# Kernel tuning notes

Measured on AMD Instinct MI355X. Metric: run time of the kernel, lower is better.

## Reference

```python
import jax, jax.numpy as jnp
import numpy as np

GRANULARITY = 50
PERCENTILES = (0.01, 0.99)


def setup_inputs() -> dict:
    key = jax.random.key(0)
    H = W = 6144
    sp = jax.random.uniform(key, (H, W), dtype=jnp.float32)
    return {
        "signal_probabilities": sp,
        "rho_max": jnp.float32(H - 1),
        "rho_min": jnp.float32(0.0),
        "theta_min_horizontal": jnp.float32(0.01),
        "theta_max_horizontal": jnp.float32(0.05),
        "theta_min_vertical": jnp.float32(1.52),
        "theta_max_vertical": jnp.float32(1.56),
    }


def _linspace(a, b, n):
    t = jnp.arange(n, dtype=jnp.float32) / (n - 1)
    return a + (b - a) * t


def _fix_edge_effects(buf):
    buf = buf.at[0, :].set(buf[1, :])
    buf = buf.at[-1, :].set(buf[-2, :])
    buf = buf.at[:, 0].set(buf[:, 1])
    buf = buf.at[:, -1].set(buf[:, -2])
    return buf


def _fill_buffer(H, W, thetas, rhos, mode):
    # vectorized over all granularity lines at once (no python loop over lines)
    if mode == "horizontal":
        y = jnp.arange(H)
        # x[g, H]: x = -y*tan(theta) + rho/cos(theta)
        x = -y[None, :] * jnp.tan(thetas)[:, None] + (rhos / jnp.cos(thetas))[:, None]
        x = jnp.clip(jnp.round(x).astype(jnp.int32), 0, W - 1)
        yb = jnp.broadcast_to(y[None, :], x.shape)
        buf = jnp.zeros((H, W), jnp.int32).at[yb, x].add(1)
        buf = jnp.cumsum(buf, axis=1)
    else:
        x = jnp.arange(W)
        # y[g, W]: y = -x/tan(theta) + rho/sin(theta)
        y = -x[None, :] / jnp.tan(thetas)[:, None] + (rhos / jnp.sin(thetas))[:, None]
        y = jnp.clip(jnp.round(y).astype(jnp.int32), 0, H - 1)
        xb = jnp.broadcast_to(x[None, :], y.shape)
        buf = jnp.zeros((H, W), jnp.int32).at[y, xb].add(1)
        buf = jnp.cumsum(buf, axis=0)
    return _fix_edge_effects(buf)


def _get_bounds(nsp, thetas, rhos, mode):
    g = GRANULARITY
    H, W = nsp.shape
    buf = _fill_buffer(H, W, thetas, rhos, mode)
    # segment-sum replaces the dense one_hot * probs reduction (same math)
    values = jax.ops.segment_sum(nsp.reshape(-1), buf.reshape(-1), num_segments=g)
    c = jnp.cumsum(values) / jnp.sum(values)
    lower = jnp.argmax(c >= PERCENTILES[0])  # first index with cumsum >= p0
    upper = (g - 1) - jnp.argmax((c <= PERCENTILES[1])[::-1]) + 2  # last index with cumsum <= p1, +2
    return lower, upper


def _take_neg(a, i):
    # a[-i] with python-style negative indexing (i == 0 -> a[0])
    g = a.shape[0]
    return jnp.take(a, (g - i) % g)


def _intersect(r1, t1, r2, t2):
    det = jnp.cos(t1) * jnp.sin(t2) - jnp.cos(t2) * jnp.sin(t1)
    x = (r1 * jnp.sin(t2) - r2 * jnp.sin(t1)) / det
    y = (r2 * jnp.cos(t1) - r1 * jnp.cos(t2)) / det
    return jnp.stack((x, y))


def reference(signal_probabilities, rho_max, rho_min, theta_min_horizontal,
              theta_max_horizontal, theta_min_vertical, theta_max_vertical):
    g = GRANULARITY
    nsp = signal_probabilities - signal_probabilities.min()
    nsp = nsp / nsp.sum()
    rhos = _linspace(rho_max, rho_min, g)
    th = _linspace(theta_min_horizontal, theta_max_horizontal, g)
    tv = _linspace(theta_min_vertical, theta_max_vertical, g)
    lh, uh = _get_bounds(nsp, th, rhos, "horizontal")
    lv, uv = _get_bounds(nsp, tv, rhos, "vertical")
    r_min_h, r_max_h = _take_neg(rhos, lh), _take_neg(rhos, uh)
    t_min_h, t_max_h = _take_neg(th, lh), _take_neg(th, uh)
    r_min_v, r_max_v = _take_neg(rhos, lv), _take_neg(rhos, uv)
    t_min_v, t_max_v = _take_neg(tv, lv), _take_neg(tv, uv)
    # [top-left, top-right, bottom-right, bottom-left] -> shape (4, 2)
    return jnp.stack([
        _intersect(r_min_h, t_min_h, r_min_v, t_min_v),
        _intersect(r_max_h, t_max_h, r_min_v, t_min_v),
        _intersect(r_max_h, t_max_h, r_max_v, t_max_v),
        _intersect(r_min_h, t_min_h, r_max_v, t_max_v),
    ], axis=0)
```

## Files before the change

### kernel.cpp

```cpp
#include <hip/hip_runtime.h>
#include <math.h>

#define HH 6144
#define WW 6144
constexpr int G = 50;
constexpr int NCOPY = 64;
constexpr int NG = NCOPY * G;
constexpr int BIG = 0x0FFFFFFF;
constexpr int C0 = 4 * NG + NCOPY;


__device__ inline void ldsAddF(float* p, float v)      { __hip_atomic_fetch_add(p, v, __ATOMIC_RELAXED, __HIP_MEMORY_SCOPE_WORKGROUP); }
__device__ inline void ldsAddU(unsigned* p, unsigned v){ __hip_atomic_fetch_add(p, v, __ATOMIC_RELAXED, __HIP_MEMORY_SCOPE_WORKGROUP); }
__device__ inline void glbAddF(float* p, float v)      { __hip_atomic_fetch_add(p, v, __ATOMIC_RELAXED, __HIP_MEMORY_SCOPE_AGENT); }
__device__ inline void glbAddU(unsigned* p, unsigned v){ __hip_atomic_fetch_add(p, v, __ATOMIC_RELAXED, __HIP_MEMORY_SCOPE_AGENT); }

__global__ void crop_init(unsigned int* __restrict__ ws,
                          const float* __restrict__ p_rmax,
                          const float* __restrict__ p_rmin,
                          const float* __restrict__ p_thmin,
                          const float* __restrict__ p_thmax,
                          const float* __restrict__ p_tvmin,
                          const float* __restrict__ p_tvmax) {
  int i = blockIdx.x * 256 + threadIdx.x;
  if (i < 4 * NG) ws[i] = 0u;
  else if (i < 4 * NG + NCOPY) ws[i] = 0x7F800000u;

  if (blockIdx.x == 0 && threadIdx.x < G) {
    int t = threadIdx.x;
    double u    = (double)t / (double)(G - 1);
    double rmax = (double)p_rmax[0], rmin = (double)p_rmin[0];
    double rho  = rmax + (rmin - rmax) * u;
    double th   = (double)p_thmin[0] + ((double)p_thmax[0] - (double)p_thmin[0]) * u;
    double tv   = (double)p_tvmin[0] + ((double)p_tvmax[0] - (double)p_tvmin[0]) * u;
    double* dT  = (double*)(ws + C0);
    double* dRC = (double*)(ws + C0 + 100);
    float*  fva = (float*)(ws + C0 + 200);
    float*  fvb = (float*)(ws + C0 + 250);
    dT[t]  = tan(th);
    dRC[t] = rho / cos(th);
    fva[t] = (float)(rho / sin(tv));
    fvb[t] = (float)(cos(tv) / sin(tv));
  }
}

__launch_bounds__(384)
__global__ void crop_main(const float* __restrict__ sp,
                          float* __restrict__ wsf) {
  __shared__ int pxh[G], pxv[G];
  __shared__ float hsum[G + 1], vsum[G + 1];
  __shared__ unsigned int hcnt[G + 1], vcnt[G + 1];
  __shared__ float wmin[6];

  const int t  = threadIdx.x;
  const int y  = blockIdx.x;
  const int yp = min(max(y, 1), HH - 2);
  const float fyp = (float)yp;

  const int x0 = t * 16;
  const float4* p4 = (const float4*)(sp + (size_t)y * WW + x0);
  float4 q0 = p4[0], q1 = p4[1], q2 = p4[2], q3 = p4[3];

  for (int i = t; i < G + 1; i += 384) { hsum[i] = 0.f; vsum[i] = 0.f; hcnt[i] = 0u; vcnt[i] = 0u; }

  if (t < G) {
    const unsigned int* wsu = (const unsigned int*)wsf;
    const double* dT  = (const double*)(wsu + C0);
    const double* dRC = (const double*)(wsu + C0 + 100);
    const float*  fva = (const float*)(wsu + C0 + 200);
    const float*  fvb = (const float*)(wsu + C0 + 250);

    double xg = rint(fma(-(double)yp, dT[t], dRC[t]));
    xg = fmin(fmax(xg, 0.0), (double)(WW - 1));
    int xi = (int)xg;
    pxh[t] = (xi <= 1) ? 0 : (xi >= WW - 1 ? BIG : xi);

    float va = fva[t], vb = fvb[t];
    int lo = 1, hi = WW - 1;
    while (lo < hi) {
      int m = (lo + hi) >> 1;
      float yv = rintf(fmaf(-(float)m, vb, va));
      yv = fminf(fmaxf(yv, 0.f), (float)(HH - 1));
      if (yv <= fyp) hi = m; else lo = m + 1;
    }
    pxv[t] = (lo >= WW - 1) ? BIG : (lo == 1 ? 0 : lo);
  }
  __syncthreads();

  float px[16] = { q0.x,q0.y,q0.z,q0.w, q1.x,q1.y,q1.z,q1.w,
                   q2.x,q2.y,q2.z,q2.w, q3.x,q3.y,q3.z,q3.w };

  int lo = 0, hi = G;
  while (lo < hi) { int m = (lo + hi) >> 1; if (pxh[m] <= x0) hi = m; else lo = m + 1; }
  const int lbh = lo;
  const int nbh = (lbh > 0) ? pxh[lbh - 1] : BIG;
  const int kh  = min(nbh - x0, 16);

  lo = 0; hi = G;
  while (lo < hi) { int m = (lo + hi) >> 1; if (pxv[m] <= x0) hi = m; else lo = m + 1; }
  const int lbv = lo;
  const int nbv = (lbv > 0) ? pxv[lbv - 1] : BIG;
  const int kv  = min(nbv - x0, 16);

  const int sh = G - lbh, sv = G - lbv;

  float S = 0.f, Ah = 0.f, Av = 0.f, mn = 3.4e38f;
#pragma unroll
  for (int k = 0; k < 16; ++k) {
    float v = px[k];
    mn = fminf(mn, v);
    S += v;
    if (k + 1 == kh) Ah = S;
    if (k + 1 == kv) Av = S;
  }

  ldsAddF(&hsum[sh], Ah); ldsAddU(&hcnt[sh], (unsigned)kh);
  if (kh < 16) { ldsAddF(&hsum[sh + 1], S - Ah); ldsAddU(&hcnt[sh + 1], (unsigned)(16 - kh)); }
  ldsAddF(&vsum[sv], Av); ldsAddU(&vcnt[sv], (unsigned)kv);
  if (kv < 16) { ldsAddF(&vsum[sv + 1], S - Av); ldsAddU(&vcnt[sv + 1], (unsigned)(16 - kv)); }

  float m = mn;
  for (int off = 32; off; off >>= 1) m = fminf(m, __shfl_down(m, off));
  if ((t & 63) == 0) wmin[t >> 6] = m;
  __syncthreads();

  const int copy = blockIdx.x & (NCOPY - 1);
  unsigned int* wsu = (unsigned int*)wsf;
  if (t == 0) {
    float mm = wmin[0];
    for (int i = 1; i < 6; ++i) mm = fminf(mm, wmin[i]);
    atomicMin(&wsu[4 * NG + copy], __float_as_uint(mm));
  }
  if (t < G) {
    glbAddF(&wsf[copy * G + t], hsum[t]);
    glbAddU(&wsu[2 * NG + copy * G + t], hcnt[t]);
  } else if (t >= 64 && t < 64 + G) {
    int s = t - 64;
    glbAddF(&wsf[NG + copy * G + s], vsum[s]);
    glbAddU(&wsu[3 * NG + copy * G + s], vcnt[s]);
  }
}

__launch_bounds__(512)
__global__ void crop_final(const float* __restrict__ wsf,
                           const float* __restrict__ p_rmax,
                           const float* __restrict__ p_rmin,
                           const float* __restrict__ p_thmin,
                           const float* __restrict__ p_thmax,
                           const float* __restrict__ p_tvmin,
                           const float* __restrict__ p_tvmax,
                           float* __restrict__ out) {
  __shared__ double psum[100][4];
  __shared__ unsigned int pcnt[100][4];
  __shared__ double val[100];
  __shared__ float  sminv;
  const unsigned int* wsu = (const unsigned int*)wsf;
  const int t = threadIdx.x;

  if (t < 64) {
    float v = __uint_as_float(wsu[4 * NG + t]);
    for (int off = 32; off; off >>= 1) v = fminf(v, __shfl_down(v, off));
    if (t == 0) sminv = v;
  }

  if (t < 400) {
    const int pair = t >> 2, chunk = t & 3;
    const int fam = pair >= G;
    const int g = fam ? pair - G : pair;
    const int sumBase = fam ? NG : 0;
    const int cntBase = (2 + fam) * NG;
    double s = 0.0; unsigned int c = 0;
#pragma unroll
    for (int i = 0; i < 16; ++i) {
      const int copy = chunk * 16 + i;
      s += (double)wsf[sumBase + copy * G + g];
      c += wsu[cntBase + copy * G + g];
    }
    psum[pair][chunk] = s;
    pcnt[pair][chunk] = c;
  }
  __syncthreads();

  if (t < 100) {
    double s = psum[t][0] + psum[t][1] + psum[t][2] + psum[t][3];
    double c = (double)(pcnt[t][0] + pcnt[t][1] + pcnt[t][2] + pcnt[t][3]);
    val[t] = s - (double)sminv * c;
  }
  __syncthreads();

  if (t == 0) {
    double rmax = p_rmax[0], rmin = p_rmin[0];
    double thmin = p_thmin[0], thmax = p_thmax[0];
    double tvmin = p_tvmin[0], tvmax = p_tvmax[0];

    auto bounds = [&](const double* v, int& lowerI, int& upperI) {
      double tot = 0;
      for (int s = 0; s < G; ++s) tot += v[s];
      double c = 0; bool found = false; int last = -1; lowerI = 0;
      for (int s = 0; s < G; ++s) {
        c += v[s];
        double cc = c / tot;
        if (!found && cc >= 0.01) { lowerI = s; found = true; }
        if (cc <= 0.99) last = s;
      }
      upperI = (last < 0) ? (G + 1) : (last + 2);
    };
    int lh, uh, lv, uv;
    bounds(&val[0], lh, uh);
    bounds(&val[G], lv, uv);

    auto tn  = [&](int i) { return ((G - i) % G + G) % G; };
    auto rho = [&](int i) { double u = (double)i / (G - 1); return rmax + (rmin - rmax) * u; };
    auto thf = [&](int i) { double u = (double)i / (G - 1); return thmin + (thmax - thmin) * u; };
    auto tvf = [&](int i) { double u = (double)i / (G - 1); return tvmin + (tvmax - tvmin) * u; };

    int ihmin = tn(lh), ihmax = tn(uh), ivmin = tn(lv), ivmax = tn(uv);
    double r_min_h = rho(ihmin), t_min_h = thf(ihmin);
    double r_max_h = rho(ihmax), t_max_h = thf(ihmax);
    double r_min_v = rho(ivmin), t_min_v = tvf(ivmin);
    double r_max_v = rho(ivmax), t_max_v = tvf(ivmax);

    auto inter = [&](double r1, double t1, double r2, double t2, float* o) {
      double det = cos(t1) * sin(t2) - cos(t2) * sin(t1);
      o[0] = (float)((r1 * sin(t2) - r2 * sin(t1)) / det);
      o[1] = (float)((r2 * cos(t1) - r1 * cos(t2)) / det);
    };
    inter(r_min_h, t_min_h, r_min_v, t_min_v, out + 0);
    inter(r_max_h, t_max_h, r_min_v, t_min_v, out + 2);
    inter(r_max_h, t_max_h, r_max_v, t_max_v, out + 4);
    inter(r_min_h, t_min_h, r_max_v, t_max_v, out + 6);
  }
}

extern "C" void kernel_launch(void* const* d_in, const int* in_sizes, int n_in,
                              void* d_out, int out_size, void* d_ws, size_t ws_size,
                              hipStream_t stream) {
  const float* sp    = (const float*)d_in[0];
  const float* rmax  = (const float*)d_in[1];
  const float* rmin  = (const float*)d_in[2];
  const float* thmin = (const float*)d_in[3];
  const float* thmax = (const float*)d_in[4];
  const float* tvmin = (const float*)d_in[5];
  const float* tvmax = (const float*)d_in[6];
  float* wsf = (float*)d_ws;
  float* outp = (float*)d_out;

  const int initN = 4 * NG + NCOPY;
  crop_init<<<(initN + 255) / 256, 256, 0, stream>>>((unsigned int*)d_ws,
                                                     rmax, rmin, thmin, thmax, tvmin, tvmax);
  crop_main<<<HH, 384, 0, stream>>>(sp, wsf);
  crop_final<<<1, 512, 0, stream>>>(wsf, rmax, rmin, thmin, thmax, tvmin, tvmax, outp);
}
```

Baseline: 247.8 us.

## Fuse final reduction into main kernel via last-block counter, two rows per block

```diff
diff --git a/kernel.cpp b/kernel.cpp
--- a/kernel.cpp
+++ b/kernel.cpp
@@ -7,13 +7,22 @@
 constexpr int NCOPY = 64;
 constexpr int NG = NCOPY * G;
 constexpr int BIG = 0x0FFFFFFF;
-constexpr int C0 = 4 * NG + NCOPY;
-
+constexpr int MINBASE = 4 * NG;
+constexpr int CTR = MINBASE + NCOPY;
+constexpr int C0 = CTR + 2;
+
+constexpr int ROWS = 2;
+constexpr int TPR  = 256;
+constexpr int TPB  = ROWS * TPR;
+constexpr int PXT  = WW / TPR;
+constexpr int NBLK = HH / ROWS;
 
 __device__ inline void ldsAddF(float* p, float v)      { __hip_atomic_fetch_add(p, v, __ATOMIC_RELAXED, __HIP_MEMORY_SCOPE_WORKGROUP); }
 __device__ inline void ldsAddU(unsigned* p, unsigned v){ __hip_atomic_fetch_add(p, v, __ATOMIC_RELAXED, __HIP_MEMORY_SCOPE_WORKGROUP); }
 __device__ inline void glbAddF(float* p, float v)      { __hip_atomic_fetch_add(p, v, __ATOMIC_RELAXED, __HIP_MEMORY_SCOPE_AGENT); }
 __device__ inline void glbAddU(unsigned* p, unsigned v){ __hip_atomic_fetch_add(p, v, __ATOMIC_RELAXED, __HIP_MEMORY_SCOPE_AGENT); }
+__device__ inline float atomLoadF(const float* p)      { return __hip_atomic_load(p, __ATOMIC_RELAXED, __HIP_MEMORY_SCOPE_AGENT); }
+__device__ inline unsigned atomLoadU(const unsigned* p){ return __hip_atomic_load(p, __ATOMIC_RELAXED, __HIP_MEMORY_SCOPE_AGENT); }
 
 __global__ void crop_init(unsigned int* __restrict__ ws,
                           const float* __restrict__ p_rmax,
@@ -23,8 +32,9 @@
                           const float* __restrict__ p_tvmin,
                           const float* __restrict__ p_tvmax) {
   int i = blockIdx.x * 256 + threadIdx.x;
-  if (i < 4 * NG) ws[i] = 0u;
-  else if (i < 4 * NG + NCOPY) ws[i] = 0x7F800000u;
+  if (i < MINBASE) ws[i] = 0u;
+  else if (i < MINBASE + NCOPY) ws[i] = 0x7F800000u;
+  else if (i < C0) ws[i] = 0u;
 
   if (blockIdx.x == 0 && threadIdx.x < G) {
     int t = threadIdx.x;
@@ -33,80 +43,101 @@
     double rho  = rmax + (rmin - rmax) * u;
     double th   = (double)p_thmin[0] + ((double)p_thmax[0] - (double)p_thmin[0]) * u;
     double tv   = (double)p_tvmin[0] + ((double)p_tvmax[0] - (double)p_tvmin[0]) * u;
-    double* dT  = (double*)(ws + C0);
-    double* dRC = (double*)(ws + C0 + 100);
-    float*  fva = (float*)(ws + C0 + 200);
-    float*  fvb = (float*)(ws + C0 + 250);
+    double cth = cos(th), sth = sin(th);
+    double ctv = cos(tv), stv = sin(tv);
+    double* dT   = (double*)(ws + C0);
+    double* dRC  = (double*)(ws + C0 + 100);
+    float*  fva  = (float*)(ws + C0 + 200);
+    float*  fvb  = (float*)(ws + C0 + 250);
+    double* dRho = (double*)(ws + C0 + 300);
+    double* dSth = (double*)(ws + C0 + 400);
+    double* dCth = (double*)(ws + C0 + 500);
+    double* dStv = (double*)(ws + C0 + 600);
+    double* dCtv = (double*)(ws + C0 + 700);
     dT[t]  = tan(th);
-    dRC[t] = rho / cos(th);
-    fva[t] = (float)(rho / sin(tv));
-    fvb[t] = (float)(cos(tv) / sin(tv));
+    dRC[t] = rho / cth;
+    fva[t] = (float)(rho / stv);
+    fvb[t] = (float)(ctv / stv);
+    dRho[t] = rho; dSth[t] = sth; dCth[t] = cth; dStv[t] = stv; dCtv[t] = ctv;
   }
 }
 
-__launch_bounds__(384)
+__launch_bounds__(TPB)
 __global__ void crop_main(const float* __restrict__ sp,
-                          float* __restrict__ wsf) {
-  __shared__ int pxh[G], pxv[G];
+                          float* __restrict__ wsf,
+                          float* __restrict__ out) {
+  __shared__ int pxh[ROWS][G], pxv[ROWS][G];
   __shared__ float hsum[G + 1], vsum[G + 1];
   __shared__ unsigned int hcnt[G + 1], vcnt[G + 1];
-  __shared__ float wmin[6];
-
-  const int t  = threadIdx.x;
-  const int y  = blockIdx.x;
-  const int yp = min(max(y, 1), HH - 2);
-  const float fyp = (float)yp;
-
-  const int x0 = t * 16;
+  __shared__ float wmin[TPB / 64];
+  __shared__ int lastFlag;
+  __shared__ double psum[100][4];
+  __shared__ unsigned int pcnt[100][4];
+  __shared__ double val[100];
+  __shared__ float sminv;
+
+  const int t   = threadIdx.x;
+  const int bid = blockIdx.x;
+  const int r   = t / TPR;
+  const int tt  = t - r * TPR;
+  const int y   = bid * ROWS + r;
+  const int yp  = min(max(y, 1), HH - 2);
+  const int x0  = tt * PXT;
+
   const float4* p4 = (const float4*)(sp + (size_t)y * WW + x0);
-  float4 q0 = p4[0], q1 = p4[1], q2 = p4[2], q3 = p4[3];
-
-  for (int i = t; i < G + 1; i += 384) { hsum[i] = 0.f; vsum[i] = 0.f; hcnt[i] = 0u; vcnt[i] = 0u; }
-
-  if (t < G) {
-    const unsigned int* wsu = (const unsigned int*)wsf;
+  float4 q0 = p4[0], q1 = p4[1], q2 = p4[2], q3 = p4[3], q4 = p4[4], q5 = p4[5];
+
+  for (int i = t; i < G + 1; i += TPB) { hsum[i] = 0.f; vsum[i] = 0.f; hcnt[i] = 0u; vcnt[i] = 0u; }
+
+  const unsigned int* wsu = (const unsigned int*)wsf;
+  if (t < 2 * G) {
+    const int rr = (t >= G) ? 1 : 0;
+    const int g  = t - rr * G;
+    const int yq = min(max(bid * ROWS + rr, 1), HH - 2);
+    const float fyq = (float)yq;
     const double* dT  = (const double*)(wsu + C0);
     const double* dRC = (const double*)(wsu + C0 + 100);
     const float*  fva = (const float*)(wsu + C0 + 200);
     const float*  fvb = (const float*)(wsu + C0 + 250);
 
-    double xg = rint(fma(-(double)yp, dT[t], dRC[t]));
+    double xg = rint(fma(-(double)yq, dT[g], dRC[g]));
     xg = fmin(fmax(xg, 0.0), (double)(WW - 1));
     int xi = (int)xg;
-    pxh[t] = (xi <= 1) ? 0 : (xi >= WW - 1 ? BIG : xi);
-
-    float va = fva[t], vb = fvb[t];
+    pxh[rr][g] = (xi <= 1) ? 0 : (xi >= WW - 1 ? BIG : xi);
+
+    float va = fva[g], vb = fvb[g];
     int lo = 1, hi = WW - 1;
     while (lo < hi) {
       int m = (lo + hi) >> 1;
       float yv = rintf(fmaf(-(float)m, vb, va));
       yv = fminf(fmaxf(yv, 0.f), (float)(HH - 1));
-      if (yv <= fyp) hi = m; else lo = m + 1;
+      if (yv <= fyq) hi = m; else lo = m + 1;
     }
-    pxv[t] = (lo >= WW - 1) ? BIG : (lo == 1 ? 0 : lo);
-  }
-  __syncthreads();
-
-  float px[16] = { q0.x,q0.y,q0.z,q0.w, q1.x,q1.y,q1.z,q1.w,
-                   q2.x,q2.y,q2.z,q2.w, q3.x,q3.y,q3.z,q3.w };
+    pxv[rr][g] = (lo >= WW - 1) ? BIG : (lo == 1 ? 0 : lo);
+  }
+  __syncthreads();
+
+  float px[PXT] = { q0.x,q0.y,q0.z,q0.w, q1.x,q1.y,q1.z,q1.w,
+                    q2.x,q2.y,q2.z,q2.w, q3.x,q3.y,q3.z,q3.w,
+                    q4.x,q4.y,q4.z,q4.w, q5.x,q5.y,q5.z,q5.w };
 
   int lo = 0, hi = G;
-  while (lo < hi) { int m = (lo + hi) >> 1; if (pxh[m] <= x0) hi = m; else lo = m + 1; }
+  while (lo < hi) { int m = (lo + hi) >> 1; if (pxh[r][m] <= x0) hi = m; else lo = m + 1; }
   const int lbh = lo;
-  const int nbh = (lbh > 0) ? pxh[lbh - 1] : BIG;
-  const int kh  = min(nbh - x0, 16);
+  const int nbh = (lbh > 0) ? pxh[r][lbh - 1] : BIG;
+  const int kh  = min(nbh - x0, PXT);
 
   lo = 0; hi = G;
-  while (lo < hi) { int m = (lo + hi) >> 1; if (pxv[m] <= x0) hi = m; else lo = m + 1; }
+  while (lo < hi) { int m = (lo + hi) >> 1; if (pxv[r][m] <= x0) hi = m; else lo = m + 1; }
   const int lbv = lo;
-  const int nbv = (lbv > 0) ? pxv[lbv - 1] : BIG;
-  const int kv  = min(nbv - x0, 16);
+  const int nbv = (lbv > 0) ? pxv[r][lbv - 1] : BIG;
+  const int kv  = min(nbv - x0, PXT);
 
   const int sh = G - lbh, sv = G - lbv;
 
   float S = 0.f, Ah = 0.f, Av = 0.f, mn = 3.4e38f;
 #pragma unroll
-  for (int k = 0; k < 16; ++k) {
+  for (int k = 0; k < PXT; ++k) {
     float v = px[k];
     mn = fminf(mn, v);
     S += v;
@@ -115,54 +146,44 @@
   }
 
   ldsAddF(&hsum[sh], Ah); ldsAddU(&hcnt[sh], (unsigned)kh);
-  if (kh < 16) { ldsAddF(&hsum[sh + 1], S - Ah); ldsAddU(&hcnt[sh + 1], (unsigned)(16 - kh)); }
+  if (kh < PXT) { ldsAddF(&hsum[sh + 1], S - Ah); ldsAddU(&hcnt[sh + 1], (unsigned)(PXT - kh)); }
   ldsAddF(&vsum[sv], Av); ldsAddU(&vcnt[sv], (unsigned)kv);
-  if (kv < 16) { ldsAddF(&vsum[sv + 1], S - Av); ldsAddU(&vcnt[sv + 1], (unsigned)(16 - kv)); }
+  if (kv < PXT) { ldsAddF(&vsum[sv + 1], S - Av); ldsAddU(&vcnt[sv + 1], (unsigned)(PXT - kv)); }
 
   float m = mn;
   for (int off = 32; off; off >>= 1) m = fminf(m, __shfl_down(m, off));
   if ((t & 63) == 0) wmin[t >> 6] = m;
   __syncthreads();
 
-  const int copy = blockIdx.x & (NCOPY - 1);
-  unsigned int* wsu = (unsigned int*)wsf;
+  const int copy = bid & (NCOPY - 1);
+  unsigned int* wsw = (unsigned int*)wsf;
   if (t == 0) {
     float mm = wmin[0];
-    for (int i = 1; i < 6; ++i) mm = fminf(mm, wmin[i]);
-    atomicMin(&wsu[4 * NG + copy], __float_as_uint(mm));
+    for (int i = 1; i < TPB / 64; ++i) mm = fminf(mm, wmin[i]);
+    atomicMin(&wsw[MINBASE + copy], __float_as_uint(mm));
   }
   if (t < G) {
     glbAddF(&wsf[copy * G + t], hsum[t]);
-    glbAddU(&wsu[2 * NG + copy * G + t], hcnt[t]);
+    glbAddU(&wsw[2 * NG + copy * G + t], hcnt[t]);
   } else if (t >= 64 && t < 64 + G) {
     int s = t - 64;
     glbAddF(&wsf[NG + copy * G + s], vsum[s]);
-    glbAddU(&wsu[3 * NG + copy * G + s], vcnt[s]);
-  }
-}
-
-__launch_bounds__(512)
-__global__ void crop_final(const float* __restrict__ wsf,
-                           const float* __restrict__ p_rmax,
-                           const float* __restrict__ p_rmin,
-                           const float* __restrict__ p_thmin,
-                           const float* __restrict__ p_thmax,
-                           const float* __restrict__ p_tvmin,
-                           const float* __restrict__ p_tvmax,
-                           float* __restrict__ out) {
-  __shared__ double psum[100][4];
-  __shared__ unsigned int pcnt[100][4];
-  __shared__ double val[100];
-  __shared__ float  sminv;
-  const unsigned int* wsu = (const unsigned int*)wsf;
-  const int t = threadIdx.x;
+    glbAddU(&wsw[3 * NG + copy * G + s], vcnt[s]);
+  }
+
+  __syncthreads();
+  if (t == 0) {
+    unsigned prev = __hip_atomic_fetch_add(&wsw[CTR], 1u, __ATOMIC_ACQ_REL, __HIP_MEMORY_SCOPE_AGENT);
+    lastFlag = (prev == (unsigned)(NBLK - 1));
+  }
+  __syncthreads();
+  if (!lastFlag) return;
 
   if (t < 64) {
-    float v = __uint_as_float(wsu[4 * NG + t]);
+    float v = __uint_as_float(atomLoadU(&wsu[MINBASE + t]));
     for (int off = 32; off; off >>= 1) v = fminf(v, __shfl_down(v, off));
     if (t == 0) sminv = v;
   }
-
   if (t < 400) {
     const int pair = t >> 2, chunk = t & 3;
     const int fam = pair >= G;
@@ -172,9 +193,9 @@
     double s = 0.0; unsigned int c = 0;
 #pragma unroll
     for (int i = 0; i < 16; ++i) {
-      const int copy = chunk * 16 + i;
-      s += (double)wsf[sumBase + copy * G + g];
-      c += wsu[cntBase + copy * G + g];
+      const int cp = chunk * 16 + i;
+      s += (double)atomLoadF(&wsf[sumBase + cp * G + g]);
+      c += atomLoadU(&wsu[cntBase + cp * G + g]);
     }
     psum[pair][chunk] = s;
     pcnt[pair][chunk] = c;
@@ -189,10 +210,6 @@
   __syncthreads();
 
   if (t == 0) {
-    double rmax = p_rmax[0], rmin = p_rmin[0];
-    double thmin = p_thmin[0], thmax = p_thmax[0];
-    double tvmin = p_tvmin[0], tvmax = p_tvmax[0];
-
     auto bounds = [&](const double* v, int& lowerI, int& upperI) {
       double tot = 0;
       for (int s = 0; s < G; ++s) tot += v[s];
@@ -209,26 +226,26 @@
     bounds(&val[0], lh, uh);
     bounds(&val[G], lv, uv);
 
-    auto tn  = [&](int i) { return ((G - i) % G + G) % G; };
-    auto rho = [&](int i) { double u = (double)i / (G - 1); return rmax + (rmin - rmax) * u; };
-    auto thf = [&](int i) { double u = (double)i / (G - 1); return thmin + (thmax - thmin) * u; };
-    auto tvf = [&](int i) { double u = (double)i / (G - 1); return tvmin + (tvmax - tvmin) * u; };
-
+    const double* dRho = (const double*)(wsu + C0 + 300);
+    const double* dSth = (const double*)(wsu + C0 + 400);
+    const double* dCth = (const double*)(wsu + C0 + 500);
+    const double* dStv = (const double*)(wsu + C0 + 600);
+    const double* dCtv = (const double*)(wsu + C0 + 700);
+
+    auto tn = [&](int i) { return ((G - i) % G + G) % G; };
     int ihmin = tn(lh), ihmax = tn(uh), ivmin = tn(lv), ivmax = tn(uv);
-    double r_min_h = rho(ihmin), t_min_h = thf(ihmin);
-    double r_max_h = rho(ihmax), t_max_h = thf(ihmax);
-    double r_min_v = rho(ivmin), t_min_v = tvf(ivmin);
-    double r_max_v = rho(ivmax), t_max_v = tvf(ivmax);
-
-    auto inter = [&](double r1, double t1, double r2, double t2, float* o) {
-      double det = cos(t1) * sin(t2) - cos(t2) * sin(t1);
-      o[0] = (float)((r1 * sin(t2) - r2 * sin(t1)) / det);
-      o[1] = (float)((r2 * cos(t1) - r1 * cos(t2)) / det);
+
+    auto inter = [&](int ih, int iv, float* o) {
+      double r1 = dRho[ih], s1 = dSth[ih], c1 = dCth[ih];
+      double r2 = dRho[iv], s2 = dStv[iv], c2 = dCtv[iv];
+      double det = c1 * s2 - c2 * s1;
+      o[0] = (float)((r1 * s2 - r2 * s1) / det);
+      o[1] = (float)((r2 * c1 - r1 * c2) / det);
     };
-    inter(r_min_h, t_min_h, r_min_v, t_min_v, out + 0);
-    inter(r_max_h, t_max_h, r_min_v, t_min_v, out + 2);
-    inter(r_max_h, t_max_h, r_max_v, t_max_v, out + 4);
-    inter(r_min_h, t_min_h, r_max_v, t_max_v, out + 6);
+    inter(ihmin, ivmin, out + 0);
+    inter(ihmax, ivmin, out + 2);
+    inter(ihmax, ivmax, out + 4);
+    inter(ihmin, ivmax, out + 6);
   }
 }
 
@@ -242,12 +259,10 @@
   const float* thmax = (const float*)d_in[4];
   const float* tvmin = (const float*)d_in[5];
   const float* tvmax = (const float*)d_in[6];
-  float* wsf = (float*)d_ws;
+  float* wsf  = (float*)d_ws;
   float* outp = (float*)d_out;
 
-  const int initN = 4 * NG + NCOPY;
-  crop_init<<<(initN + 255) / 256, 256, 0, stream>>>((unsigned int*)d_ws,
-                                                     rmax, rmin, thmin, thmax, tvmin, tvmax);
-  crop_main<<<HH, 384, 0, stream>>>(sp, wsf);
-  crop_final<<<1, 512, 0, stream>>>(wsf, rmax, rmin, thmin, thmax, tvmin, tvmax, outp);
+  crop_init<<<(C0 + 255) / 256, 256, 0, stream>>>((unsigned int*)d_ws,
+                                                  rmax, rmin, thmin, thmax, tvmin, tvmax);
+  crop_main<<<NBLK, TPB, 0, stream>>>(sp, wsf, outp);
 }
```

Measured after the change: 399.5 us. 1.61x slower.
